# Kernel optimization log

Measured on AMD Instinct MI355X. Metric: run time of the kernel, lower is better.

Reference implementation:

```python
import jax, jax.numpy as jnp
import numpy as np

B, LQ, LKV, D, H = 4, 1024, 2048, 1024, 16
HD = D // H
EPS = 1e-5
NEG = -1e9


def _layernorm(x, w, b):
    mu = jnp.mean(x, axis=-1, keepdims=True)
    var = jnp.mean(jnp.square(x - mu), axis=-1, keepdims=True)
    return (x - mu) * jax.lax.rsqrt(var + EPS) * w + b


def setup_inputs() -> dict:
    key = jax.random.key(0)
    ks = jax.random.split(key, 10)
    q = jax.random.normal(ks[0], (B, LQ, D), dtype=jnp.float32)
    kv = jax.random.normal(ks[1], (B, LKV, D), dtype=jnp.float32)
    # ragged kv lengths; mask True == padding
    lengths = jax.random.randint(ks[2], (B,), LKV // 4, LKV + 1)
    mask = jnp.arange(LKV)[None, :] >= lengths[:, None]  # [B, LKV] bool
    s = 1.0 / np.sqrt(D)
    params = dict(
        norm_q_w=jnp.ones((D,), jnp.float32),
        norm_q_b=jnp.zeros((D,), jnp.float32),
        norm_kv_w=jnp.ones((D,), jnp.float32),
        norm_kv_b=jnp.zeros((D,), jnp.float32),
        Wq=jax.random.normal(ks[3], (D, D), jnp.float32) * s,
        bq=jnp.zeros((D,), jnp.float32),
        Wkv=jax.random.normal(ks[4], (2 * D, D), jnp.float32) * s,
        bkv=jnp.zeros((2 * D,), jnp.float32),
        Wo=jax.random.normal(ks[5], (D, D), jnp.float32) * s,
        bo=jnp.zeros((D,), jnp.float32),
    )
    return dict(q=q, kv=kv, mask=mask, **params)


def reference(q, kv, mask, norm_q_w, norm_q_b, norm_kv_w, norm_kv_b, Wq, bq, Wkv, bkv, Wo, bo):
    q_res = q
    qn = _layernorm(q, norm_q_w, norm_q_b)
    kvn = _layernorm(kv, norm_kv_w, norm_kv_b)
    # projections
    qh = (qn @ Wq.T + bq).reshape(B, LQ, H, HD)
    kvp = (kvn @ Wkv.T + bkv).reshape(B, LKV, 2, H, HD)
    k, v = kvp[:, :, 0], kvp[:, :, 1]  # [B, LKV, H, HD]
    # masked cross attention (math-equivalent to varlen flash attn over unpadded kv)
    scale = 1.0 / np.sqrt(HD)
    scores = jnp.einsum('bqhd,bkhd->bhqk', qh, k) * scale
    scores = jnp.where(mask[:, None, None, :], NEG, scores)
    attn = jax.nn.softmax(scores, axis=-1)
    out = jnp.einsum('bhqk,bkhd->bqhd', attn, v).reshape(B, LQ, D)
    # out proj + residual (dropout is identity in eval)
    return q_res + (out @ Wo.T + bo)


if __name__ == '__main__':
    inp = setup_inputs()
    y = reference(**inp)
    print(y.shape, y.dtype)
```

## Files before the change

### kernel.cpp

```cpp
#include <hip/hip_runtime.h>

#define DEV __device__ __forceinline__

typedef unsigned short u16;
typedef float  floatx4 __attribute__((ext_vector_type(4)));
typedef unsigned int uintx4 __attribute__((ext_vector_type(4)));
typedef __bf16 bf16x8 __attribute__((ext_vector_type(8)));

constexpr int cB = 4, cLQ = 1024, cLKV = 2048, cD = 1024, cH = 16, cHD = 64;

DEV u16 f2bf(float f) {
  unsigned u = __builtin_bit_cast(unsigned, f);
  u += 0x7fffu + ((u >> 16) & 1u);
  return (u16)(u >> 16);
}

DEV u16 f2bf_t(float f) {
  return (u16)(__builtin_bit_cast(unsigned, f) >> 16);
}

DEV bf16x8 ld_frag(const u16* p) {
  uintx4 u = *(const uintx4*)p;
  return __builtin_bit_cast(bf16x8, u);
}

DEV floatx4 mfma16(bf16x8 a, bf16x8 b, floatx4 c) {
  return __builtin_amdgcn_mfma_f32_16x16x32_bf16(a, b, c, 0, 0, 0);
}

DEV float ex2(float x) { return __builtin_amdgcn_exp2f(x); }

__global__ __launch_bounds__(256) void prep_kernel(
    const float* __restrict__ q, const float* __restrict__ kv,
    const float* __restrict__ nqw, const float* __restrict__ nqb,
    const float* __restrict__ nkw, const float* __restrict__ nkb,
    u16* __restrict__ qn, u16* __restrict__ kvn,
    const float* __restrict__ Wq, const float* __restrict__ Wkv,
    const float* __restrict__ Wo, u16* __restrict__ wqb,
    u16* __restrict__ wkvb, u16* __restrict__ wob,
    const void* __restrict__ mask, int* __restrict__ lens) {
  int bid = blockIdx.x, tid = threadIdx.x;
  if (bid < cB * (cLQ + cLKV)) {
    const float* x; const float* w; const float* b; u16* dst;
    if (bid < cB * cLQ) {
      x = q + (size_t)bid * cD; w = nqw; b = nqb; dst = qn + (size_t)bid * cD;
    } else {
      int r2 = bid - cB * cLQ;
      x = kv + (size_t)r2 * cD; w = nkw; b = nkb; dst = kvn + (size_t)r2 * cD;
    }
    float4 v = ((const float4*)x)[tid];
    __shared__ float sbuf[8];
    float s = v.x + v.y + v.z + v.w;
    #pragma unroll
    for (int m = 1; m < 64; m <<= 1) s += __shfl_xor(s, m, 64);
    if ((tid & 63) == 0) sbuf[tid >> 6] = s;
    __syncthreads();
    float mean = (sbuf[0] + sbuf[1] + sbuf[2] + sbuf[3]) * (1.f / cD);
    float dx = v.x - mean, dy = v.y - mean, dz = v.z - mean, dw = v.w - mean;
    float ss = dx * dx + dy * dy + dz * dz + dw * dw;
    #pragma unroll
    for (int m = 1; m < 64; m <<= 1) ss += __shfl_xor(ss, m, 64);
    if ((tid & 63) == 0) sbuf[4 + (tid >> 6)] = ss;
    __syncthreads();
    float var = (sbuf[4] + sbuf[5] + sbuf[6] + sbuf[7]) * (1.f / cD);
    float rs = rsqrtf(var + 1e-5f);
    float4 wv = ((const float4*)w)[tid];
    float4 bv = ((const float4*)b)[tid];
    ushort4 o;
    o.x = f2bf(dx * rs * wv.x + bv.x);
    o.y = f2bf(dy * rs * wv.y + bv.y);
    o.z = f2bf(dz * rs * wv.z + bv.z);
    o.w = f2bf(dw * rs * wv.w + bv.w);
    ((ushort4*)dst)[tid] = o;
  } else if (bid < cB * (cLQ + cLKV) + 4096) {
    int gi = (bid - cB * (cLQ + cLKV)) * 256 + tid;
    const float* src; u16* dst; int off;
    if (gi < 262144)      { src = Wq;  dst = wqb;  off = gi; }
    else if (gi < 786432) { src = Wkv; dst = wkvb; off = gi - 262144; }
    else                  { src = Wo;  dst = wob;  off = gi - 786432; }
    float4 v = ((const float4*)src)[off];
    ushort4 o;
    o.x = f2bf(v.x); o.y = f2bf(v.y); o.z = f2bf(v.z); o.w = f2bf(v.w);
    ((ushort4*)dst)[off] = o;
  } else {
    __shared__ int smode;
    __shared__ int cnt[cB];
    if (tid == 0) smode = 0;
    if (tid < cB) cnt[tid] = 0;
    __syncthreads();
    const unsigned* mi = (const unsigned*)mask;
    int bad = 0;
    for (int i = tid; i < cB * cLKV / 4; i += 256)
      if (mi[i] > 1u) bad = 1;
    if (bad) smode = 1;
    __syncthreads();
    if (smode == 0) {
      for (int b = 0; b < cB; b++) {
        int c = 0;
        for (int i = tid; i < cLKV; i += 256) c += (mi[(size_t)b * cLKV + i] == 0u);
        atomicAdd(&cnt[b], c);
      }
    } else {
      const unsigned char* m8 = (const unsigned char*)mask;
      for (int b = 0; b < cB; b++) {
        int c = 0;
        for (int i = tid; i < cLKV; i += 256) c += (m8[(size_t)b * cLKV + i] == 0);
        atomicAdd(&cnt[b], c);
      }
    }
    __syncthreads();
    if (tid < cB) lens[tid] = cnt[tid];
  }
}

struct TileCtx {
  int m16, quad, wr, wc;
};

DEV void gemm_mainloop(const u16* __restrict__ A, const u16* __restrict__ Bm,
                       int row0, int col0, int K, u16* As, u16* Bs,
                       const TileCtx& t, floatx4 (&acc)[4][4]) {
  int tid = threadIdx.x;
  int wave = tid >> 6, lane = tid & 63;
  int srow = wave * 16 + (lane >> 2);
  int sseg = (lane & 3) * 8;
  const u16* ga = A + (size_t)(row0 + srow) * K + sseg;
  const u16* gb = Bm + (size_t)(col0 + srow) * K + sseg;
  const size_t rstep = (size_t)64 * K;
  int woff = srow * 32 + sseg;

  uintx4 a0 = *(const uintx4*)ga;
  uintx4 a1 = *(const uintx4*)(ga + rstep);
  uintx4 b0 = *(const uintx4*)gb;
  uintx4 b1 = *(const uintx4*)(gb + rstep);
  *(uintx4*)(As + woff) = a0;
  *(uintx4*)(As + woff + 2048) = a1;
  *(uintx4*)(Bs + woff) = b0;
  *(uintx4*)(Bs + woff + 2048) = b1;
  a0 = *(const uintx4*)(ga + 32);
  a1 = *(const uintx4*)(ga + rstep + 32);
  b0 = *(const uintx4*)(gb + 32);
  b1 = *(const uintx4*)(gb + rstep + 32);
  __syncthreads();

  for (int k0 = 0; k0 < K; k0 += 32) {
    int cur = (k0 >> 5) & 1;
    const u16* rA = As + cur * 4096;
    const u16* rB = Bs + cur * 4096;
    bf16x8 af[4], bfr[4];
    #pragma unroll
    for (int i = 0; i < 4; i++)
      af[i] = ld_frag(&rA[(t.wr * 64 + i * 16 + t.m16) * 32 + t.quad * 8]);
    #pragma unroll
    for (int j = 0; j < 4; j++)
      bfr[j] = ld_frag(&rB[(t.wc * 64 + j * 16 + t.m16) * 32 + t.quad * 8]);
    if (k0 + 32 < K) {
      u16* nA = As + (cur ^ 1) * 4096 + woff;
      u16* nB = Bs + (cur ^ 1) * 4096 + woff;
      *(uintx4*)nA = a0;
      *(uintx4*)(nA + 2048) = a1;
      *(uintx4*)nB = b0;
      *(uintx4*)(nB + 2048) = b1;
      if (k0 + 64 < K) {
        a0 = *(const uintx4*)(ga + k0 + 64);
        a1 = *(const uintx4*)(ga + rstep + k0 + 64);
        b0 = *(const uintx4*)(gb + k0 + 64);
        b1 = *(const uintx4*)(gb + rstep + k0 + 64);
      }
    }
    #pragma unroll
    for (int i = 0; i < 4; i++)
      #pragma unroll
      for (int j = 0; j < 4; j++)
        acc[i][j] = mfma16(af[i], bfr[j], acc[i][j]);
    __syncthreads();
  }
}

__global__ __launch_bounds__(256) void proj_fused(
    const u16* __restrict__ qn, const u16* __restrict__ wqb,
    const float* __restrict__ bq, u16* __restrict__ qhb,
    const u16* __restrict__ kvn, const u16* __restrict__ wkvb,
    const float* __restrict__ bkv, u16* __restrict__ khb,
    u16* __restrict__ vthb) {
  __shared__ __align__(16) u16 As[2 * 128 * 32];
  __shared__ __align__(16) u16 Bs[2 * 128 * 32];
  int bid = blockIdx.x;
  int lane = threadIdx.x & 63;
  TileCtx t;
  t.m16 = lane & 15; t.quad = lane >> 4;
  int wave = threadIdx.x >> 6;
  t.wr = wave >> 1; t.wc = wave & 1;

  bool isQ = bid < 256;
  int row0, col0;
  const u16* A; const u16* Bm; const float* bias;
  if (isQ) {
    row0 = (bid >> 3) * 128; col0 = (bid & 7) * 128;
    A = qn; Bm = wqb; bias = bq;
  } else {
    int b2 = bid - 256;
    row0 = (b2 >> 4) * 128; col0 = (b2 & 15) * 128;
    A = kvn; Bm = wkvb; bias = bkv;
  }

  floatx4 z = {0.f, 0.f, 0.f, 0.f};
  floatx4 acc[4][4];
  #pragma unroll
  for (int i = 0; i < 4; i++)
    #pragma unroll
    for (int j = 0; j < 4; j++) acc[i][j] = z;

  gemm_mainloop(A, Bm, row0, col0, cD, As, Bs, t, acc);

  #pragma unroll
  for (int j = 0; j < 4; j++) {
    int col = col0 + t.wc * 64 + j * 16 + t.m16;
    float bs = bias[col];
    if (isQ) {
      #pragma unroll
      for (int i = 0; i < 4; i++) {
        int crow = row0 + t.wr * 64 + i * 16 + t.quad * 4;
        #pragma unroll
        for (int r = 0; r < 4; r++)
          qhb[(size_t)(crow + r) * cD + col] =
              f2bf((acc[i][j][r] + bs) * 0.18033688f);
      }
    } else {
      bool isK = col < cD;
      int c2 = isK ? col : col - cD;
      int hh = c2 >> 6, dd = c2 & 63;
      #pragma unroll
      for (int i = 0; i < 4; i++) {
        int crow = row0 + t.wr * 64 + i * 16 + t.quad * 4;
        int bb = crow >> 11, kvp = crow & (cLKV - 1);
        if (isK) {
          u16* dst = khb + ((size_t)(bb * cH + hh) * cLKV + kvp) * 64 + dd;
          #pragma unroll
          for (int r = 0; r < 4; r++) dst[(size_t)r * 64] = f2bf(acc[i][j][r] + bs);
        } else {
          u16* dst = vthb + ((size_t)(bb * cH + hh) * 64 + dd) * cLKV + kvp;
          ushort4 o;
          o.x = f2bf(acc[i][j][0] + bs);
          o.y = f2bf(acc[i][j][1] + bs);
          o.z = f2bf(acc[i][j][2] + bs);
          o.w = f2bf(acc[i][j][3] + bs);
          *(ushort4*)dst = o;
        }
      }
    }
  }
}

__global__ __launch_bounds__(256) void gemm_o(
    const u16* __restrict__ A, const u16* __restrict__ Bm,
    const float* __restrict__ bias, const float* __restrict__ res,
    float* __restrict__ Cout, int N, int K) {
  __shared__ __align__(16) u16 As[2 * 128 * 32];
  __shared__ __align__(16) u16 Bs[2 * 128 * 32];
  int lane = threadIdx.x & 63;
  TileCtx t;
  t.m16 = lane & 15; t.quad = lane >> 4;
  int wave = threadIdx.x >> 6;
  t.wr = wave >> 1; t.wc = wave & 1;
  int row0 = blockIdx.y * 128, col0 = blockIdx.x * 128;

  floatx4 z = {0.f, 0.f, 0.f, 0.f};
  floatx4 acc[4][4];
  #pragma unroll
  for (int i = 0; i < 4; i++)
    #pragma unroll
    for (int j = 0; j < 4; j++) acc[i][j] = z;

  gemm_mainloop(A, Bm, row0, col0, K, As, Bs, t, acc);

  #pragma unroll
  for (int j = 0; j < 4; j++) {
    int col = col0 + t.wc * 64 + j * 16 + t.m16;
    float bs = bias[col];
    #pragma unroll
    for (int i = 0; i < 4; i++) {
      int crow = row0 + t.wr * 64 + i * 16 + t.quad * 4;
      #pragma unroll
      for (int r = 0; r < 4; r++) {
        size_t idx = (size_t)(crow + r) * N + col;
        Cout[idx] = acc[i][j][r] + bs + res[idx];
      }
    }
  }
}

constexpr int KS = 72;
constexpr int PS = 72;

template<bool MASK>
DEV void attn_compute(int k0, int len, const u16* __restrict__ Kt,
                      const u16* __restrict__ Vt, u16* __restrict__ psw,
                      bf16x8 qf0, bf16x8 qf1, int m16, int quad,
                      float& lsum, floatx4 (&accO)[4]) {
  floatx4 z = {0.f, 0.f, 0.f, 0.f};
  floatx4 s[4];
  #pragma unroll
  for (int t = 0; t < 4; t++) {
    bf16x8 kf0 = ld_frag(&Kt[(t * 16 + m16) * KS + quad * 8]);
    bf16x8 kf1 = ld_frag(&Kt[(t * 16 + m16) * KS + 32 + quad * 8]);
    floatx4 tt = z;
    tt = mfma16(kf0, qf0, tt);
    tt = mfma16(kf1, qf1, tt);
    s[t] = tt;
  }
  #pragma unroll
  for (int t = 0; t < 4; t++) {
    float e0, e1, e2, e3;
    if (MASK) {
      int key = k0 + t * 16 + quad * 4;
      e0 = (key     < len) ? ex2(s[t][0]) : 0.f;
      e1 = (key + 1 < len) ? ex2(s[t][1]) : 0.f;
      e2 = (key + 2 < len) ? ex2(s[t][2]) : 0.f;
      e3 = (key + 3 < len) ? ex2(s[t][3]) : 0.f;
    } else {
      e0 = ex2(s[t][0]);
      e1 = ex2(s[t][1]);
      e2 = ex2(s[t][2]);
      e3 = ex2(s[t][3]);
    }
    lsum += (e0 + e1) + (e2 + e3);
    ushort4 pk;
    pk.x = f2bf_t(e0); pk.y = f2bf_t(e1); pk.z = f2bf_t(e2); pk.w = f2bf_t(e3);
    *(ushort4*)&psw[m16 * PS + t * 16 + quad * 4] = pk;
  }
  bf16x8 ap0 = ld_frag(&psw[m16 * PS + quad * 8]);
  bf16x8 ap1 = ld_frag(&psw[m16 * PS + 32 + quad * 8]);
  #pragma unroll
  for (int db = 0; db < 4; db++) {
    bf16x8 bv0 = ld_frag(&Vt[(db * 16 + m16) * KS + quad * 8]);
    bf16x8 bv1 = ld_frag(&Vt[(db * 16 + m16) * KS + 32 + quad * 8]);
    accO[db] = mfma16(ap0, bv0, accO[db]);
    accO[db] = mfma16(ap1, bv1, accO[db]);
  }
}

__global__ __launch_bounds__(256) void attn_kernel(
    const u16* __restrict__ qh, const u16* __restrict__ kh,
    const u16* __restrict__ vth, const int* __restrict__ lens,
    u16* __restrict__ out) {
  int gid = blockIdx.x;
  int b = gid & (cB - 1);
  int h = (gid >> 2) & (cH - 1);
  int qt = gid >> 6;
  int len = lens[b];
  int wave = threadIdx.x >> 6, lane = threadIdx.x & 63;
  int m16 = lane & 15, quad = lane >> 4;

  __shared__ __align__(16) u16 Kt[64 * KS];
  __shared__ __align__(16) u16 Vt[64 * KS];
  __shared__ __align__(16) u16 Ps[4][16 * PS];
  u16* psw = &Ps[wave][0];

  int qrow = qt * 64 + wave * 16 + m16;
  const u16* qp = qh + ((size_t)(b * cLQ + qrow) * cH + h) * cHD;
  bf16x8 qf0 = ld_frag(qp + quad * 8);
  bf16x8 qf1 = ld_frag(qp + 32 + quad * 8);

  const u16* kbase = kh + (size_t)(b * cH + h) * cLKV * cHD;
  const u16* vbase = vth + (size_t)(b * cH + h) * cHD * cLKV;

  int srow = threadIdx.x >> 3;
  int sseg = threadIdx.x & 7;
  const u16* kg = kbase + (size_t)srow * cHD + sseg * 8;
  const u16* vg = vbase + (size_t)srow * cLKV + sseg * 8;

  float lsum = 0.f;
  floatx4 z = {0.f, 0.f, 0.f, 0.f};
  floatx4 accO[4] = {z, z, z, z};

  int nch = (len + 63) >> 6;
  uintx4 ka  = *(const uintx4*)kg;
  uintx4 kb2 = *(const uintx4*)(kg + (size_t)32 * cHD);
  uintx4 va  = *(const uintx4*)vg;
  uintx4 vb  = *(const uintx4*)(vg + (size_t)32 * cLKV);

  for (int c = 0; c < nch; c++) {
    int k0 = c * 64;
    __syncthreads();
    *(uintx4*)&Kt[srow * KS + sseg * 8] = ka;
    *(uintx4*)&Kt[(srow + 32) * KS + sseg * 8] = kb2;
    *(uintx4*)&Vt[srow * KS + sseg * 8] = va;
    *(uintx4*)&Vt[(srow + 32) * KS + sseg * 8] = vb;
    if (c + 1 < nch) {
      int kn = k0 + 64;
      ka  = *(const uintx4*)(kg + (size_t)kn * cHD);
      kb2 = *(const uintx4*)(kg + (size_t)(kn + 32) * cHD);
      va  = *(const uintx4*)(vg + kn);
      vb  = *(const uintx4*)(vg + (size_t)32 * cLKV + kn);
    }
    __syncthreads();
    if (k0 + 64 <= len)
      attn_compute<false>(k0, len, Kt, Vt, psw, qf0, qf1, m16, quad, lsum, accO);
    else
      attn_compute<true>(k0, len, Kt, Vt, psw, qf0, qf1, m16, quad, lsum, accO);
  }

  float tsum = lsum;
  tsum += __shfl_xor(tsum, 16, 64);
  tsum += __shfl_xor(tsum, 32, 64);

  #pragma unroll
  for (int r = 0; r < 4; r++) {
    float inv = 1.0f / __shfl(tsum, quad * 4 + r, 16);
    int qg = qt * 64 + wave * 16 + quad * 4 + r;
    size_t base = ((size_t)(b * cLQ + qg) * cH + h) * cHD;
    #pragma unroll
    for (int db = 0; db < 4; db++)
      out[base + db * 16 + m16] = f2bf(accO[db][r] * inv);
  }
}

extern "C" void kernel_launch(void* const* d_in, const int* in_sizes, int n_in,
                              void* d_out, int out_size, void* d_ws, size_t ws_size,
                              hipStream_t stream) {
  const float* q    = (const float*)d_in[0];
  const float* kv   = (const float*)d_in[1];
  const void*  mask = d_in[2];
  const float* nqw  = (const float*)d_in[3];
  const float* nqb  = (const float*)d_in[4];
  const float* nkw  = (const float*)d_in[5];
  const float* nkb  = (const float*)d_in[6];
  const float* Wq   = (const float*)d_in[7];
  const float* bq   = (const float*)d_in[8];
  const float* Wkv  = (const float*)d_in[9];
  const float* bkv  = (const float*)d_in[10];
  const float* Wo   = (const float*)d_in[11];
  const float* bo   = (const float*)d_in[12];
  float* out = (float*)d_out;

  char* w = (char*)d_ws;
  int* lens = (int*)w;       w += 256;
  u16* qn   = (u16*)w;       w += (size_t)cB * cLQ * cD * 2;
  u16* kvn  = (u16*)w;       w += (size_t)cB * cLKV * cD * 2;
  u16* wqb  = (u16*)w;       w += (size_t)cD * cD * 2;
  u16* wkvb = (u16*)w;       w += (size_t)2 * cD * cD * 2;
  u16* wob  = (u16*)w;       w += (size_t)cD * cD * 2;
  u16* qhb  = (u16*)w;       w += (size_t)cB * cLQ * cD * 2;
  u16* khb  = (u16*)w;       w += (size_t)cB * cH * cLKV * cHD * 2;
  u16* vthb = (u16*)w;       w += (size_t)cB * cH * cHD * cLKV * 2;
  u16* aob  = (u16*)w;

  prep_kernel<<<cB * (cLQ + cLKV) + 4096 + 1, 256, 0, stream>>>(
      q, kv, nqw, nqb, nkw, nkb, qn, kvn,
      Wq, Wkv, Wo, wqb, wkvb, wob, mask, lens);
  proj_fused<<<1280, 256, 0, stream>>>(
      qn, wqb, bq, qhb, kvn, wkvb, bkv, khb, vthb);
  attn_kernel<<<cB * cH * (cLQ / 64), 256, 0, stream>>>(
      qhb, khb, vthb, lens, aob);
  gemm_o<<<dim3(cD / 128, cB * cLQ / 128), 256, 0, stream>>>(
      aob, wob, bo, q, out, cD, cD);
}
```

Before: 277.2 us.

## Use direct global-to-LDS loads in GEMM and lighter barriers in attention

```diff
diff --git a/kernel.cpp b/kernel.cpp
--- a/kernel.cpp
+++ b/kernel.cpp
@@ -29,6 +29,14 @@
 }
 
 DEV float ex2(float x) { return __builtin_amdgcn_exp2f(x); }
+
+DEV void gload16(const u16* g, u16* l) {
+  __builtin_amdgcn_global_load_lds(
+      (const __attribute__((address_space(1))) void*)g,
+      (__attribute__((address_space(3))) void*)l, 16, 0, 0);
+}
+
+#define BAR_LDS() asm volatile("s_waitcnt lgkmcnt(0)\n\ts_barrier" ::: "memory")
 
 __global__ __launch_bounds__(256) void prep_kernel(
     const float* __restrict__ q, const float* __restrict__ kv,
@@ -127,24 +135,26 @@
   const u16* ga = A + (size_t)(row0 + srow) * K + sseg;
   const u16* gb = Bm + (size_t)(col0 + srow) * K + sseg;
   const size_t rstep = (size_t)64 * K;
-  int woff = srow * 32 + sseg;
-
-  uintx4 a0 = *(const uintx4*)ga;
-  uintx4 a1 = *(const uintx4*)(ga + rstep);
-  uintx4 b0 = *(const uintx4*)gb;
-  uintx4 b1 = *(const uintx4*)(gb + rstep);
-  *(uintx4*)(As + woff) = a0;
-  *(uintx4*)(As + woff + 2048) = a1;
-  *(uintx4*)(Bs + woff) = b0;
-  *(uintx4*)(Bs + woff + 2048) = b1;
-  a0 = *(const uintx4*)(ga + 32);
-  a1 = *(const uintx4*)(ga + rstep + 32);
-  b0 = *(const uintx4*)(gb + 32);
-  b1 = *(const uintx4*)(gb + rstep + 32);
+  u16* wA = As + wave * 512;
+  u16* wB = Bs + wave * 512;
+
+  gload16(ga, wA);
+  gload16(ga + rstep, wA + 2048);
+  gload16(gb, wB);
+  gload16(gb + rstep, wB + 2048);
   __syncthreads();
 
   for (int k0 = 0; k0 < K; k0 += 32) {
     int cur = (k0 >> 5) & 1;
+    if (k0 + 32 < K) {
+      int kn = k0 + 32;
+      u16* nA = wA + (cur ^ 1) * 4096;
+      u16* nB = wB + (cur ^ 1) * 4096;
+      gload16(ga + kn, nA);
+      gload16(ga + rstep + kn, nA + 2048);
+      gload16(gb + kn, nB);
+      gload16(gb + rstep + kn, nB + 2048);
+    }
     const u16* rA = As + cur * 4096;
     const u16* rB = Bs + cur * 4096;
     bf16x8 af[4], bfr[4];
@@ -154,20 +164,6 @@
     #pragma unroll
     for (int j = 0; j < 4; j++)
       bfr[j] = ld_frag(&rB[(t.wc * 64 + j * 16 + t.m16) * 32 + t.quad * 8]);
-    if (k0 + 32 < K) {
-      u16* nA = As + (cur ^ 1) * 4096 + woff;
-      u16* nB = Bs + (cur ^ 1) * 4096 + woff;
-      *(uintx4*)nA = a0;
-      *(uintx4*)(nA + 2048) = a1;
-      *(uintx4*)nB = b0;
-      *(uintx4*)(nB + 2048) = b1;
-      if (k0 + 64 < K) {
-        a0 = *(const uintx4*)(ga + k0 + 64);
-        a1 = *(const uintx4*)(ga + rstep + k0 + 64);
-        b0 = *(const uintx4*)(gb + k0 + 64);
-        b1 = *(const uintx4*)(gb + rstep + k0 + 64);
-      }
-    }
     #pragma unroll
     for (int i = 0; i < 4; i++)
       #pragma unroll
@@ -382,7 +378,7 @@
 
   for (int c = 0; c < nch; c++) {
     int k0 = c * 64;
-    __syncthreads();
+    BAR_LDS();
     *(uintx4*)&Kt[srow * KS + sseg * 8] = ka;
     *(uintx4*)&Kt[(srow + 32) * KS + sseg * 8] = kb2;
     *(uintx4*)&Vt[srow * KS + sseg * 8] = va;
@@ -394,7 +390,7 @@
       va  = *(const uintx4*)(vg + kn);
       vb  = *(const uintx4*)(vg + (size_t)32 * cLKV + kn);
     }
-    __syncthreads();
+    BAR_LDS();
     if (k0 + 64 <= len)
       attn_compute<false>(k0, len, Kt, Vt, psw, qf0, qf1, m16, quad, lsum, accO);
     else
```

After: 295.7 us. 6.7% more time.

## Double-buffer attention K/V tiles, use lighter LDS barriers, schedule longest batches first

Applied to the files above, without the earlier changes.

```diff
diff --git a/kernel.cpp b/kernel.cpp
--- a/kernel.cpp
+++ b/kernel.cpp
@@ -29,6 +29,8 @@
 }
 
 DEV float ex2(float x) { return __builtin_amdgcn_exp2f(x); }
+
+#define BAR_LDS() asm volatile("s_waitcnt lgkmcnt(0)\n\ts_barrier" ::: "memory")
 
 __global__ __launch_bounds__(256) void prep_kernel(
     const float* __restrict__ q, const float* __restrict__ kv,
@@ -110,6 +112,18 @@
     }
     __syncthreads();
     if (tid < cB) lens[tid] = cnt[tid];
+    if (tid == 0) {
+      int ord[4] = {0, 1, 2, 3};
+      #pragma unroll
+      for (int a = 0; a < 3; a++)
+        #pragma unroll
+        for (int d = 0; d < 3; d++)
+          if (cnt[ord[d]] < cnt[ord[d + 1]]) {
+            int tswap = ord[d]; ord[d] = ord[d + 1]; ord[d + 1] = tswap;
+          }
+      #pragma unroll
+      for (int a = 0; a < 4; a++) lens[4 + a] = ord[a];
+    }
   }
 }
 
@@ -141,7 +155,7 @@
   a1 = *(const uintx4*)(ga + rstep + 32);
   b0 = *(const uintx4*)(gb + 32);
   b1 = *(const uintx4*)(gb + rstep + 32);
-  __syncthreads();
+  BAR_LDS();
 
   for (int k0 = 0; k0 < K; k0 += 32) {
     int cur = (k0 >> 5) & 1;
@@ -173,7 +187,7 @@
       #pragma unroll
       for (int j = 0; j < 4; j++)
         acc[i][j] = mfma16(af[i], bfr[j], acc[i][j]);
-    __syncthreads();
+    BAR_LDS();
   }
 }
 
@@ -345,15 +359,15 @@
     const u16* __restrict__ vth, const int* __restrict__ lens,
     u16* __restrict__ out) {
   int gid = blockIdx.x;
-  int b = gid & (cB - 1);
+  int b = lens[4 + (gid & (cB - 1))];
   int h = (gid >> 2) & (cH - 1);
   int qt = gid >> 6;
   int len = lens[b];
   int wave = threadIdx.x >> 6, lane = threadIdx.x & 63;
   int m16 = lane & 15, quad = lane >> 4;
 
-  __shared__ __align__(16) u16 Kt[64 * KS];
-  __shared__ __align__(16) u16 Vt[64 * KS];
+  __shared__ __align__(16) u16 Kt[2][64 * KS];
+  __shared__ __align__(16) u16 Vt[2][64 * KS];
   __shared__ __align__(16) u16 Ps[4][16 * PS];
   u16* psw = &Ps[wave][0];
 
@@ -375,30 +389,46 @@
   floatx4 accO[4] = {z, z, z, z};
 
   int nch = (len + 63) >> 6;
-  uintx4 ka  = *(const uintx4*)kg;
-  uintx4 kb2 = *(const uintx4*)(kg + (size_t)32 * cHD);
-  uintx4 va  = *(const uintx4*)vg;
-  uintx4 vb  = *(const uintx4*)(vg + (size_t)32 * cLKV);
+  {
+    uintx4 k0a = *(const uintx4*)kg;
+    uintx4 k0b = *(const uintx4*)(kg + (size_t)32 * cHD);
+    uintx4 v0a = *(const uintx4*)vg;
+    uintx4 v0b = *(const uintx4*)(vg + (size_t)32 * cLKV);
+    *(uintx4*)&Kt[0][srow * KS + sseg * 8] = k0a;
+    *(uintx4*)&Kt[0][(srow + 32) * KS + sseg * 8] = k0b;
+    *(uintx4*)&Vt[0][srow * KS + sseg * 8] = v0a;
+    *(uintx4*)&Vt[0][(srow + 32) * KS + sseg * 8] = v0b;
+  }
+  uintx4 ka, kb2, va, vb;
+  if (nch > 1) {
+    ka  = *(const uintx4*)(kg + (size_t)64 * cHD);
+    kb2 = *(const uintx4*)(kg + (size_t)96 * cHD);
+    va  = *(const uintx4*)(vg + 64);
+    vb  = *(const uintx4*)(vg + (size_t)32 * cLKV + 64);
+  }
+  BAR_LDS();
 
   for (int c = 0; c < nch; c++) {
     int k0 = c * 64;
-    __syncthreads();
-    *(uintx4*)&Kt[srow * KS + sseg * 8] = ka;
-    *(uintx4*)&Kt[(srow + 32) * KS + sseg * 8] = kb2;
-    *(uintx4*)&Vt[srow * KS + sseg * 8] = va;
-    *(uintx4*)&Vt[(srow + 32) * KS + sseg * 8] = vb;
+    int p = c & 1;
+    if (k0 + 64 <= len)
+      attn_compute<false>(k0, len, Kt[p], Vt[p], psw, qf0, qf1, m16, quad, lsum, accO);
+    else
+      attn_compute<true>(k0, len, Kt[p], Vt[p], psw, qf0, qf1, m16, quad, lsum, accO);
     if (c + 1 < nch) {
-      int kn = k0 + 64;
-      ka  = *(const uintx4*)(kg + (size_t)kn * cHD);
-      kb2 = *(const uintx4*)(kg + (size_t)(kn + 32) * cHD);
-      va  = *(const uintx4*)(vg + kn);
-      vb  = *(const uintx4*)(vg + (size_t)32 * cLKV + kn);
-    }
-    __syncthreads();
-    if (k0 + 64 <= len)
-      attn_compute<false>(k0, len, Kt, Vt, psw, qf0, qf1, m16, quad, lsum, accO);
-    else
-      attn_compute<true>(k0, len, Kt, Vt, psw, qf0, qf1, m16, quad, lsum, accO);
+      *(uintx4*)&Kt[p ^ 1][srow * KS + sseg * 8] = ka;
+      *(uintx4*)&Kt[p ^ 1][(srow + 32) * KS + sseg * 8] = kb2;
+      *(uintx4*)&Vt[p ^ 1][srow * KS + sseg * 8] = va;
+      *(uintx4*)&Vt[p ^ 1][(srow + 32) * KS + sseg * 8] = vb;
+      if (c + 2 < nch) {
+        int kn = k0 + 128;
+        ka  = *(const uintx4*)(kg + (size_t)kn * cHD);
+        kb2 = *(const uintx4*)(kg + (size_t)(kn + 32) * cHD);
+        va  = *(const uintx4*)(vg + kn);
+        vb  = *(const uintx4*)(vg + (size_t)32 * cLKV + kn);
+      }
+    }
+    BAR_LDS();
   }
 
   float tsum = lsum;
```

New measurement: 285.8 us. +3.1%, slower.
